# Kernel optimization log

Measured on AMD Instinct MI355X. Metric: run time of the kernel, lower is better.

The kernel has to match this reference:

```python
import jax, jax.numpy as jnp
import numpy as np

INPUT_DIM, LATENT_DIM, NUM_HEADS, LATENT_RANK = 2048, 1024, 16, 256
HEAD_DIM = LATENT_DIM // NUM_HEADS


def _linear_params(key, in_dim, out_dim):
    kw, kb = jax.random.split(key)
    bound = 1.0 / np.sqrt(in_dim)
    W = jax.random.uniform(kw, (in_dim, out_dim), jnp.float32, -bound, bound)
    b = jax.random.uniform(kb, (out_dim,), jnp.float32, -bound, bound)
    return W, b


def setup_inputs() -> dict:
    key = jax.random.key(0)
    ks = jax.random.split(key, 7)
    latent = jax.random.normal(ks[0], (2, 1024, LATENT_DIM), jnp.float32)
    x = jax.random.normal(ks[1], (2, 4096, INPUT_DIM), jnp.float32)
    Wq, bq = _linear_params(ks[2], LATENT_DIM, LATENT_DIM)
    Wc, bc = _linear_params(ks[3], INPUT_DIM, LATENT_RANK)
    Wk, bk = _linear_params(ks[4], LATENT_RANK, LATENT_DIM)
    Wv, bv = _linear_params(ks[5], LATENT_RANK, LATENT_DIM)
    Wo, bo = _linear_params(ks[6], LATENT_DIM, LATENT_DIM)
    return {"latent": latent, "x": x,
            "Wq": Wq, "bq": bq, "Wc": Wc, "bc": bc,
            "Wk": Wk, "bk": bk, "Wv": Wv, "bv": bv,
            "Wo": Wo, "bo": bo}


def reference(latent, x, Wq, bq, Wc, bc, Wk, bk, Wv, bv, Wo, bo):
    B, L, _ = latent.shape
    S = x.shape[1]
    H, D = NUM_HEADS, HEAD_DIM
    Q = (latent @ Wq + bq).reshape(B, L, H, D).transpose(0, 2, 1, 3)   # (B,H,L,D)
    compressed = x @ Wc + bc                                            # (B,S,R)
    K = (compressed @ Wk + bk).reshape(B, S, H, D).transpose(0, 2, 1, 3)  # (B,H,S,D)
    V = (compressed @ Wv + bv).reshape(B, S, H, D).transpose(0, 2, 1, 3)  # (B,H,S,D)
    scores = jnp.einsum('bhld,bhsd->bhls', Q, K) / np.sqrt(D).astype(jnp.float32)
    attn_weights = jax.nn.softmax(scores, axis=-1)                      # (B,H,L,S)
    attn_out = jnp.einsum('bhls,bhsd->bhld', attn_weights, V)           # (B,H,L,D)
    attn_out = attn_out.transpose(0, 2, 1, 3).reshape(B, L, H * D)
    output = attn_out @ Wo + bo                                         # (B,L,latent_dim)
    return output, attn_weights
```

## Files before the change

kernel.cpp:

```cpp
#include <hip/hip_runtime.h>

typedef short sv8 __attribute__((ext_vector_type(8)));
typedef float fv4 __attribute__((ext_vector_type(4)));

#define MFMA16(a, b, c) __builtin_amdgcn_mfma_f32_16x16x32_bf16((a), (b), (c), 0, 0, 0)

__device__ __forceinline__ unsigned short f2bf(float f) {
    unsigned u = __builtin_bit_cast(unsigned, f);
    unsigned r = (u + 0x7FFF + ((u >> 16) & 1)) >> 16;
    return (unsigned short)r;
}

constexpr int BB = 2, LL = 1024, SS = 4096, LD = 1024, HH = 16, DD = 64;

__global__ __launch_bounds__(256) void transpose_weights(
    const float* __restrict__ Wc, const float* __restrict__ Wk, const float* __restrict__ Wv,
    const float* __restrict__ Wq, const float* __restrict__ Wo,
    unsigned short* __restrict__ Tc, unsigned short* __restrict__ Tk,
    unsigned short* __restrict__ Tv, unsigned short* __restrict__ Tq,
    unsigned short* __restrict__ To)
{
    __shared__ __align__(16) unsigned short tile[64][68];
    int bid = blockIdx.x;
    const float* W; unsigned short* T; int K, N, tix;
    if (bid < 128)      { W = Wc; T = Tc; K = 2048; N = 256;  tix = bid; }
    else if (bid < 192) { W = Wk; T = Tk; K = 256;  N = 1024; tix = bid - 128; }
    else if (bid < 256) { W = Wv; T = Tv; K = 256;  N = 1024; tix = bid - 192; }
    else if (bid < 512) { W = Wq; T = Tq; K = 1024; N = 1024; tix = bid - 256; }
    else                { W = Wo; T = To; K = 1024; N = 1024; tix = bid - 512; }
    int tn = N >> 6;
    int k0 = (tix / tn) << 6, n0 = (tix % tn) << 6;
    int t = threadIdx.x;
    int r = t >> 4, c4 = (t & 15) * 4;
#pragma unroll
    for (int i = 0; i < 4; i++) {
        int k = r + i * 16;
        float4 f = *(const float4*)(W + (size_t)(k0 + k) * N + n0 + c4);
        tile[k][c4 + 0] = f2bf(f.x); tile[k][c4 + 1] = f2bf(f.y);
        tile[k][c4 + 2] = f2bf(f.z); tile[k][c4 + 3] = f2bf(f.w);
    }
    __syncthreads();
#pragma unroll
    for (int i = 0; i < 4; i++) {
        int n = r + i * 16;
        ushort4 o;
        o.x = tile[c4 + 0][n]; o.y = tile[c4 + 1][n];
        o.z = tile[c4 + 2][n]; o.w = tile[c4 + 3][n];
        *(ushort4*)(T + (size_t)(n0 + n) * K + k0 + c4) = o;
    }
}

__global__ __launch_bounds__(256) void transpose_v(
    const unsigned short* __restrict__ V, unsigned short* __restrict__ Vt)
{
    __shared__ __align__(16) unsigned short tile[64][68];
    int s0 = blockIdx.x * 64;
    int h = blockIdx.y, b = blockIdx.z;
    int t = threadIdx.x;
    int r = t >> 4, c4 = (t & 15) * 4;
#pragma unroll
    for (int i = 0; i < 4; i++) {
        int s = r + i * 16;
        ushort4 v = *(const ushort4*)(V + (size_t)(b * SS + s0 + s) * LD + h * DD + c4);
        tile[s][c4 + 0] = v.x; tile[s][c4 + 1] = v.y;
        tile[s][c4 + 2] = v.z; tile[s][c4 + 3] = v.w;
    }
    __syncthreads();
#pragma unroll
    for (int i = 0; i < 4; i++) {
        int d = r + i * 16;
        ushort4 o;
        o.x = tile[c4 + 0][d]; o.y = tile[c4 + 1][d];
        o.z = tile[c4 + 2][d]; o.w = tile[c4 + 3][d];
        *(ushort4*)(Vt + ((size_t)(b * HH + h) * DD + d) * SS + s0 + c4) = o;
    }
}

template<int BM, int BN, bool A_F32, bool C_F32>
__global__ __launch_bounds__(256) void gemm_bias(
    const void* __restrict__ Ag, const unsigned short* __restrict__ Bt,
    const float* __restrict__ bias, void* __restrict__ Cg,
    int M, int N, int K, float scale)
{
    constexpr int LDT = 40;
    __shared__ __align__(16) unsigned short As[BM * LDT];
    __shared__ __align__(16) unsigned short Bs[BN * LDT];
    __shared__ float bias_s[BN];
    const int t = threadIdx.x;
    const int m0 = blockIdx.x * BM, n0 = blockIdx.y * BN;
    for (int i = t; i < BN; i += 256) bias_s[i] = bias[n0 + i];
    const int w = t >> 6, lane = t & 63, l15 = lane & 15, quad = lane >> 4;
    constexpr int WM = BM / 2, WN = BN / 2;
    constexpr int MT = WM / 16, NT = WN / 16;
    const int wm = (w >> 1) * WM, wn = (w & 1) * WN;
    fv4 acc[MT][NT] = {};
    const int r8 = t >> 3, c4 = (t & 7) * 4;
    for (int k0 = 0; k0 < K; k0 += 32) {
#pragma unroll
        for (int i = 0; i < BM / 32; i++) {
            int row = r8 + i * 32;
            ushort4 v;
            if constexpr (A_F32) {
                float4 f = *(const float4*)((const float*)Ag + (size_t)(m0 + row) * K + k0 + c4);
                v.x = f2bf(f.x); v.y = f2bf(f.y); v.z = f2bf(f.z); v.w = f2bf(f.w);
            } else {
                v = *(const ushort4*)((const unsigned short*)Ag + (size_t)(m0 + row) * K + k0 + c4);
            }
            *(ushort4*)&As[row * LDT + c4] = v;
        }
#pragma unroll
        for (int i = 0; i < BN / 32; i++) {
            int row = r8 + i * 32;
            ushort4 v = *(const ushort4*)(Bt + (size_t)(n0 + row) * K + k0 + c4);
            *(ushort4*)&Bs[row * LDT + c4] = v;
        }
        __syncthreads();
        sv8 af[MT], bfr[NT];
#pragma unroll
        for (int mt = 0; mt < MT; mt++)
            af[mt] = *(const sv8*)&As[(wm + mt * 16 + l15) * LDT + quad * 8];
#pragma unroll
        for (int nt = 0; nt < NT; nt++)
            bfr[nt] = *(const sv8*)&Bs[(wn + nt * 16 + l15) * LDT + quad * 8];
#pragma unroll
        for (int mt = 0; mt < MT; mt++)
#pragma unroll
            for (int nt = 0; nt < NT; nt++)
                acc[mt][nt] = MFMA16(af[mt], bfr[nt], acc[mt][nt]);
        __syncthreads();
    }
#pragma unroll
    for (int mt = 0; mt < MT; mt++) {
#pragma unroll
        for (int nt = 0; nt < NT; nt++) {
            int col = n0 + wn + nt * 16 + l15;
            float bb = bias_s[wn + nt * 16 + l15];
#pragma unroll
            for (int r = 0; r < 4; r++) {
                int row = m0 + wm + mt * 16 + quad * 4 + r;
                float vv = (acc[mt][nt][r] + bb) * scale;
                if constexpr (C_F32) ((float*)Cg)[(size_t)row * N + col] = vv;
                else ((unsigned short*)Cg)[(size_t)row * N + col] = f2bf(vv);
            }
        }
    }
}

constexpr int SC  = 128;
constexpr int KLD = 72;
constexpr int VLD = 136;

__global__ __launch_bounds__(256) void attn_kernel(
    const unsigned short* __restrict__ Qw,
    const unsigned short* __restrict__ Kw,
    const unsigned short* __restrict__ Vtw,
    float* __restrict__ Wout,
    unsigned short* __restrict__ Ow)
{
    __shared__ __align__(16) unsigned short Ks[SC * KLD];
    __shared__ __align__(16) unsigned short Vs[DD * VLD];
    __shared__ __align__(16) unsigned short Ps[4 * 16 * VLD];
    const int bid = blockIdx.x;
    const int lt = bid & 15, h = (bid >> 4) & 15, b = bid >> 8;
    const int l0 = lt * 64;
    const int t = threadIdx.x, w = t >> 6, lane = t & 63, l15 = lane & 15, quad = lane >> 4;

    const unsigned short* qrow = Qw + (size_t)(b * LL + l0 + w * 16 + l15) * LD + h * DD;
    const sv8 aq0 = *(const sv8*)(qrow + quad * 8);
    const sv8 aq1 = *(const sv8*)(qrow + 32 + quad * 8);

    const unsigned short* kg0 = Kw + (size_t)(b * SS) * LD + h * DD;
    const int kr = t >> 3, kc = (t & 7) * 8;

    float lsum[4] = {0.f, 0.f, 0.f, 0.f};
    sv8 kreg[4];
#pragma unroll
    for (int i = 0; i < 4; i++)
        kreg[i] = *(const sv8*)(kg0 + (size_t)(kr + i * 32) * LD + kc);
    for (int s0 = 0; s0 < SS; s0 += SC) {
#pragma unroll
        for (int i = 0; i < 4; i++)
            *(sv8*)&Ks[(kr + i * 32) * KLD + kc] = kreg[i];
        __syncthreads();
        if (s0 + SC < SS) {
            const unsigned short* kg = kg0 + (size_t)(s0 + SC) * LD;
#pragma unroll
            for (int i = 0; i < 4; i++)
                kreg[i] = *(const sv8*)(kg + (size_t)(kr + i * 32) * LD + kc);
        }
#pragma unroll
        for (int c = 0; c < 8; c++) {
            sv8 b0 = *(const sv8*)&Ks[(c * 16 + l15) * KLD + quad * 8];
            sv8 b1 = *(const sv8*)&Ks[(c * 16 + l15) * KLD + 32 + quad * 8];
            fv4 sc = {0.f, 0.f, 0.f, 0.f};
            __builtin_amdgcn_s_setprio(1);
            sc = MFMA16(aq0, b0, sc);
            sc = MFMA16(aq1, b1, sc);
            __builtin_amdgcn_s_setprio(0);
#pragma unroll
            for (int r = 0; r < 4; r++) lsum[r] += __expf(sc[r]);
        }
        __syncthreads();
    }
    float inv_l[4];
#pragma unroll
    for (int r = 0; r < 4; r++) {
        float v = lsum[r];
        v += __shfl_xor(v, 1); v += __shfl_xor(v, 2);
        v += __shfl_xor(v, 4); v += __shfl_xor(v, 8);
        inv_l[r] = 1.0f / v;
    }

    fv4 oacc[4] = {};
    float* wbase = Wout + ((size_t)((b * HH + h) * LL + l0 + w * 16)) * SS;
    const unsigned short* vg0 = Vtw + (size_t)(b * HH + h) * DD * SS;
    const int vd = t >> 4, vc = (t & 15) * 8;
    sv8 vreg[4];
#pragma unroll
    for (int i = 0; i < 4; i++)
        kreg[i] = *(const sv8*)(kg0 + (size_t)(kr + i * 32) * LD + kc);
#pragma unroll
    for (int i = 0; i < 4; i++)
        vreg[i] = *(const sv8*)(vg0 + (size_t)(vd + i * 16) * SS + vc);
    for (int s0 = 0; s0 < SS; s0 += SC) {
#pragma unroll
        for (int i = 0; i < 4; i++)
            *(sv8*)&Ks[(kr + i * 32) * KLD + kc] = kreg[i];
#pragma unroll
        for (int i = 0; i < 4; i++)
            *(sv8*)&Vs[(vd + i * 16) * VLD + vc] = vreg[i];
        __syncthreads();
        if (s0 + SC < SS) {
            const unsigned short* kg = kg0 + (size_t)(s0 + SC) * LD;
#pragma unroll
            for (int i = 0; i < 4; i++)
                kreg[i] = *(const sv8*)(kg + (size_t)(kr + i * 32) * LD + kc);
#pragma unroll
            for (int i = 0; i < 4; i++)
                vreg[i] = *(const sv8*)(vg0 + (size_t)(vd + i * 16) * SS + s0 + SC + vc);
        }
        float* wp0 = wbase + s0;
#pragma unroll
        for (int c = 0; c < 8; c++) {
            sv8 b0 = *(const sv8*)&Ks[(c * 16 + l15) * KLD + quad * 8];
            sv8 b1 = *(const sv8*)&Ks[(c * 16 + l15) * KLD + 32 + quad * 8];
            fv4 sc = {0.f, 0.f, 0.f, 0.f};
            __builtin_amdgcn_s_setprio(1);
            sc = MFMA16(aq0, b0, sc);
            sc = MFMA16(aq1, b1, sc);
            __builtin_amdgcn_s_setprio(0);
#pragma unroll
            for (int r = 0; r < 4; r++) {
                float wv = __expf(sc[r]) * inv_l[r];
                wp0[(size_t)(quad * 4 + r) * SS + c * 16 + l15] = wv;
                Ps[(w * 16 + quad * 4 + r) * VLD + c * 16 + l15] = f2bf(wv);
            }
        }
        sv8 ap[4];
#pragma unroll
        for (int ks = 0; ks < 4; ks++)
            ap[ks] = *(const sv8*)&Ps[(w * 16 + l15) * VLD + ks * 32 + quad * 8];
        __builtin_amdgcn_s_setprio(1);
#pragma unroll
        for (int dt = 0; dt < 4; dt++)
#pragma unroll
            for (int ks = 0; ks < 4; ks++) {
                sv8 bv = *(const sv8*)&Vs[(dt * 16 + l15) * VLD + ks * 32 + quad * 8];
                oacc[dt] = MFMA16(ap[ks], bv, oacc[dt]);
            }
        __builtin_amdgcn_s_setprio(0);
        __syncthreads();
    }
    unsigned short* obase = Ow + (size_t)(b * LL + l0 + w * 16) * LD + h * DD;
#pragma unroll
    for (int dt = 0; dt < 4; dt++)
#pragma unroll
        for (int r = 0; r < 4; r++)
            obase[(size_t)(quad * 4 + r) * LD + dt * 16 + l15] = f2bf(oacc[dt][r]);
}

extern "C" void kernel_launch(void* const* d_in, const int* in_sizes, int n_in,
                              void* d_out, int out_size, void* d_ws, size_t ws_size,
                              hipStream_t stream) {
    const float* latent = (const float*)d_in[0];
    const float* x      = (const float*)d_in[1];
    const float* Wq = (const float*)d_in[2];
    const float* bq = (const float*)d_in[3];
    const float* Wc = (const float*)d_in[4];
    const float* bc = (const float*)d_in[5];
    const float* Wk = (const float*)d_in[6];
    const float* bk = (const float*)d_in[7];
    const float* Wv = (const float*)d_in[8];
    const float* bv = (const float*)d_in[9];
    const float* Wo = (const float*)d_in[10];
    const float* bo = (const float*)d_in[11];

    float* out   = (float*)d_out;
    float* attnw = out + (size_t)2 * 1024 * 1024;

    char* ws = (char*)d_ws;
    size_t off = 0;
    auto alloc = [&](size_t bytes) -> void* {
        void* p = ws + off; off += (bytes + 255) & ~(size_t)255; return p;
    };
    unsigned short* Tc   = (unsigned short*)alloc((size_t)2048 * 256 * 2);
    unsigned short* Tk   = (unsigned short*)alloc((size_t)1024 * 256 * 2);
    unsigned short* Tv   = (unsigned short*)alloc((size_t)1024 * 256 * 2);
    unsigned short* Tq   = (unsigned short*)alloc((size_t)1024 * 1024 * 2);
    unsigned short* To   = (unsigned short*)alloc((size_t)1024 * 1024 * 2);
    unsigned short* comp = (unsigned short*)alloc((size_t)8192 * 256 * 2);
    unsigned short* Kws  = (unsigned short*)alloc((size_t)8192 * 1024 * 2);
    unsigned short* Vws  = (unsigned short*)alloc((size_t)8192 * 1024 * 2);
    unsigned short* Vtws = (unsigned short*)alloc((size_t)8192 * 1024 * 2);
    unsigned short* Qws  = (unsigned short*)alloc((size_t)2048 * 1024 * 2);
    unsigned short* Ows  = (unsigned short*)alloc((size_t)2048 * 1024 * 2);

    transpose_weights<<<768, 256, 0, stream>>>(Wc, Wk, Wv, Wq, Wo, Tc, Tk, Tv, Tq, To);
    gemm_bias<128, 64, true, false><<<dim3(64, 4), 256, 0, stream>>>(
        x, Tc, bc, comp, 8192, 256, 2048, 1.0f);
    gemm_bias<128, 128, false, false><<<dim3(64, 8), 256, 0, stream>>>(
        comp, Tk, bk, Kws, 8192, 1024, 256, 1.0f);
    gemm_bias<128, 128, false, false><<<dim3(64, 8), 256, 0, stream>>>(
        comp, Tv, bv, Vws, 8192, 1024, 256, 1.0f);
    gemm_bias<64, 128, true, false><<<dim3(32, 8), 256, 0, stream>>>(
        latent, Tq, bq, Qws, 2048, 1024, 1024, 0.125f);
    transpose_v<<<dim3(64, 16, 2), 256, 0, stream>>>(Vws, Vtws);
    attn_kernel<<<512, 256, 0, stream>>>(Qws, Kws, Vtws, attnw, Ows);
    gemm_bias<64, 128, false, true><<<dim3(32, 8), 256, 0, stream>>>(
        Ows, To, bo, out, 2048, 1024, 1024, 1.0f);
}
```

Before: 891.1 us.

## Pre-convert inputs to bf16 and register-prefetch next K tile in GEMM

```diff
diff --git a/kernel.cpp b/kernel.cpp
--- a/kernel.cpp
+++ b/kernel.cpp
@@ -12,6 +12,25 @@
 }
 
 constexpr int BB = 2, LL = 1024, SS = 4096, LD = 1024, HH = 16, DD = 64;
+
+constexpr size_t NX = (size_t)2 * 4096 * 2048;
+constexpr size_t NL = (size_t)2 * 1024 * 1024;
+
+__global__ __launch_bounds__(256) void convert_inputs(
+    const float* __restrict__ x, const float* __restrict__ latent,
+    unsigned short* __restrict__ xb, unsigned short* __restrict__ lb)
+{
+    size_t i = ((size_t)blockIdx.x * 256 + threadIdx.x) * 8;
+    const float* src; unsigned short* dst;
+    if (i < NX) { src = x + i; dst = xb + i; }
+    else        { size_t j = i - NX; src = latent + j; dst = lb + j; }
+    float4 a = *(const float4*)src;
+    float4 b = *(const float4*)(src + 4);
+    ushort4 o0 = {f2bf(a.x), f2bf(a.y), f2bf(a.z), f2bf(a.w)};
+    ushort4 o1 = {f2bf(b.x), f2bf(b.y), f2bf(b.z), f2bf(b.w)};
+    *(ushort4*)dst = o0;
+    *(ushort4*)(dst + 4) = o1;
+}
 
 __global__ __launch_bounds__(256) void transpose_weights(
     const float* __restrict__ Wc, const float* __restrict__ Wk, const float* __restrict__ Wv,
@@ -76,9 +95,9 @@
     }
 }
 
-template<int BM, int BN, bool A_F32, bool C_F32>
+template<int BM, int BN, bool C_F32>
 __global__ __launch_bounds__(256) void gemm_bias(
-    const void* __restrict__ Ag, const unsigned short* __restrict__ Bt,
+    const unsigned short* __restrict__ Ag, const unsigned short* __restrict__ Bt,
     const float* __restrict__ bias, void* __restrict__ Cg,
     int M, int N, int K, float scale)
 {
@@ -94,27 +113,29 @@
     constexpr int MT = WM / 16, NT = WN / 16;
     const int wm = (w >> 1) * WM, wn = (w & 1) * WN;
     fv4 acc[MT][NT] = {};
-    const int r8 = t >> 3, c4 = (t & 7) * 4;
+    const int r4 = t >> 2, c8 = (t & 3) * 8;
+    constexpr int AI = BM / 64, BI = BN / 64;
+    const unsigned short* Aptr = Ag + (size_t)(m0 + r4) * K + c8;
+    const unsigned short* Bptr = Bt + (size_t)(n0 + r4) * K + c8;
+    sv8 areg[AI], breg[BI];
+#pragma unroll
+    for (int i = 0; i < AI; i++) areg[i] = *(const sv8*)(Aptr + (size_t)(i * 64) * K);
+#pragma unroll
+    for (int i = 0; i < BI; i++) breg[i] = *(const sv8*)(Bptr + (size_t)(i * 64) * K);
     for (int k0 = 0; k0 < K; k0 += 32) {
 #pragma unroll
-        for (int i = 0; i < BM / 32; i++) {
-            int row = r8 + i * 32;
-            ushort4 v;
-            if constexpr (A_F32) {
-                float4 f = *(const float4*)((const float*)Ag + (size_t)(m0 + row) * K + k0 + c4);
-                v.x = f2bf(f.x); v.y = f2bf(f.y); v.z = f2bf(f.z); v.w = f2bf(f.w);
-            } else {
-                v = *(const ushort4*)((const unsigned short*)Ag + (size_t)(m0 + row) * K + k0 + c4);
-            }
-            *(ushort4*)&As[row * LDT + c4] = v;
-        }
-#pragma unroll
-        for (int i = 0; i < BN / 32; i++) {
-            int row = r8 + i * 32;
-            ushort4 v = *(const ushort4*)(Bt + (size_t)(n0 + row) * K + k0 + c4);
-            *(ushort4*)&Bs[row * LDT + c4] = v;
-        }
-        __syncthreads();
+        for (int i = 0; i < AI; i++) *(sv8*)&As[(r4 + i * 64) * LDT + c8] = areg[i];
+#pragma unroll
+        for (int i = 0; i < BI; i++) *(sv8*)&Bs[(r4 + i * 64) * LDT + c8] = breg[i];
+        __syncthreads();
+        if (k0 + 32 < K) {
+#pragma unroll
+            for (int i = 0; i < AI; i++)
+                areg[i] = *(const sv8*)(Aptr + (size_t)(i * 64) * K + k0 + 32);
+#pragma unroll
+            for (int i = 0; i < BI; i++)
+                breg[i] = *(const sv8*)(Bptr + (size_t)(i * 64) * K + k0 + 32);
+        }
         sv8 af[MT], bfr[NT];
 #pragma unroll
         for (int mt = 0; mt < MT; mt++)
@@ -315,17 +336,21 @@
     unsigned short* Qws  = (unsigned short*)alloc((size_t)2048 * 1024 * 2);
     unsigned short* Ows  = (unsigned short*)alloc((size_t)2048 * 1024 * 2);
 
+    unsigned short* xb = Kws;
+    unsigned short* lb = Ows;
+
+    convert_inputs<<<9216, 256, 0, stream>>>(x, latent, xb, lb);
     transpose_weights<<<768, 256, 0, stream>>>(Wc, Wk, Wv, Wq, Wo, Tc, Tk, Tv, Tq, To);
-    gemm_bias<128, 64, true, false><<<dim3(64, 4), 256, 0, stream>>>(
-        x, Tc, bc, comp, 8192, 256, 2048, 1.0f);
-    gemm_bias<128, 128, false, false><<<dim3(64, 8), 256, 0, stream>>>(
+    gemm_bias<128, 64, false><<<dim3(64, 4), 256, 0, stream>>>(
+        xb, Tc, bc, comp, 8192, 256, 2048, 1.0f);
+    gemm_bias<64, 128, false><<<dim3(32, 8), 256, 0, stream>>>(
+        lb, Tq, bq, Qws, 2048, 1024, 1024, 0.125f);
+    gemm_bias<128, 128, false><<<dim3(64, 8), 256, 0, stream>>>(
         comp, Tk, bk, Kws, 8192, 1024, 256, 1.0f);
-    gemm_bias<128, 128, false, false><<<dim3(64, 8), 256, 0, stream>>>(
+    gemm_bias<128, 128, false><<<dim3(64, 8), 256, 0, stream>>>(
         comp, Tv, bv, Vws, 8192, 1024, 256, 1.0f);
-    gemm_bias<64, 128, true, false><<<dim3(32, 8), 256, 0, stream>>>(
-        latent, Tq, bq, Qws, 2048, 1024, 1024, 0.125f);
     transpose_v<<<dim3(64, 16, 2), 256, 0, stream>>>(Vws, Vtws);
     attn_kernel<<<512, 256, 0, stream>>>(Qws, Kws, Vtws, attnw, Ows);
-    gemm_bias<64, 128, false, true><<<dim3(32, 8), 256, 0, stream>>>(
+    gemm_bias<64, 128, true><<<dim3(32, 8), 256, 0, stream>>>(
         Ows, To, bo, out, 2048, 1024, 1024, 1.0f);
 }
```

Result: faster. 842.8 us (-5.4%).
